# Kernel optimization log

Hardware: AMD Instinct MI355X
Metric: run time of the kernel (lower is better)

Reference implementation:

```python
import jax, jax.numpy as jnp
import numpy as np
from jax import lax

H = 512
W = 512
KS = 9  # dilation and Gaussian kernel size
# OpenCV: sigma=0 -> sigma = 0.3*((ksize-1)*0.5 - 1) + 0.8 = 1.7 for ksize=9
_SIGMA = 0.3 * ((KS - 1) * 0.5 - 1.0) + 0.8
_g = np.exp(-0.5 * ((np.arange(KS) - (KS - 1) / 2.0) / _SIGMA) ** 2)
_g = (_g / _g.sum()).astype(np.float32)
GAUSS = jnp.asarray(_g)


def setup_inputs() -> dict:
    key = jax.random.key(0)
    k1, k2, k3 = jax.random.split(key, 3)
    B, N = 64, 13860
    eye = jnp.eye(4, dtype=jnp.float32)
    # near-identity camera matrices so points project on-screen
    V = eye + 0.02 * jax.random.normal(k1, (B, 4, 4), jnp.float32)
    P = eye + 0.02 * jax.random.normal(k2, (B, 4, 4), jnp.float32)
    xyz = jax.random.uniform(k3, (N, 3), jnp.float32, -0.9, 0.9)
    pts = jnp.concatenate([xyz, jnp.ones((N, 1), jnp.float32)], axis=1)
    return {"V_matrix": V, "P_matrix": P, "raw_base_points": pts}


def reference(V_matrix, P_matrix, raw_base_points):
    B = V_matrix.shape[0]
    VP = jnp.einsum('bij,bjk->bik', P_matrix, V_matrix)          # [B,4,4]
    tp = jnp.einsum('ni,bji->bnj', raw_base_points, VP)          # points @ VP^T -> [B,N,4]
    w = tp[..., 3:4]
    xyz = jnp.where(w != 0, tp[..., :3] / w, tp[..., :3])       # perspective divide
    sx = jnp.round((xyz[..., 0] + 1.0) * 0.5 * W).astype(jnp.int32)
    sy = jnp.round((1.0 - (xyz[..., 1] + 1.0) * 0.5) * H).astype(jnp.int32)
    valid = (sx >= 0) & (sx < W) & (sy >= 0) & (sy < H)
    flat = jnp.where(valid, sy * W + sx, -1)                     # -1 -> dropped by scatter

    def splat(f):  # point splat: 255 at hit pixels (this is the inverted image)
        return jnp.zeros(H * W, jnp.float32).at[f].set(255.0, mode='drop').reshape(H, W)

    img = jax.vmap(splat)(flat)                                  # [B,H,W] in {0,255}
    dil = lax.reduce_window(img, -jnp.inf, lax.max, (1, KS, KS), (1, 1, 1), 'SAME')
    # 9x9 Gaussian blur, separable, BORDER_REFLECT_101 (OpenCV default)
    pad = jnp.pad(dil, ((0, 0), (KS // 2, KS // 2), (KS // 2, KS // 2)), mode='reflect')
    x = pad[:, None]                                             # [B,1,H+8,W+8]
    sm = lax.conv_general_dilated(x, GAUSS.reshape(1, 1, KS, 1), (1, 1), 'VALID')
    sm = lax.conv_general_dilated(sm, GAUSS.reshape(1, 1, 1, KS), (1, 1), 'VALID')[:, 0]
    # threshold(smoothed > 100) -> 255, then /255 -> {0,1}
    mask = (jnp.round(sm) > 100.0).astype(jnp.float32)           # [B,H,W]
    return jnp.broadcast_to(mask[:, None], (B, 3, H, W))
```

## Files before the change

kernel.cpp:

```cpp
#include <hip/hip_runtime.h>
#include <math.h>
#include <stdint.h>

#define HH 512
#define WW 512
#define BB 64
#define NP 13860
#define WPR 16
#define IMG_WORDS (BB * HH * WPR)

struct GaussW { float g[9]; };

__device__ __forceinline__ int reflect_idx(int i) {
    if (i < 0) i = -i;
    if (i > 511) i = 1022 - i;
    return i;
}

__global__ __launch_bounds__(256)
void zero_kernel(uint4* __restrict__ p) {
    p[blockIdx.x * 256 + threadIdx.x] = make_uint4(0u, 0u, 0u, 0u);
}

__global__ __launch_bounds__(256)
void splat_kernel(const float* __restrict__ V,
                  const float* __restrict__ P,
                  const float* __restrict__ pts,
                  unsigned int* __restrict__ gbm) {
    __shared__ float VP[4][4];
    const int b = blockIdx.y;
    const int t = threadIdx.x;
    if (t < 16) {
        const int i = t >> 2, k = t & 3;
        const float* Pb = P + b * 16;
        const float* Vb = V + b * 16;
        float a = __fmul_rn(Pb[i*4+0], Vb[0*4+k]);
        a = __fmaf_rn(Pb[i*4+1], Vb[1*4+k], a);
        a = __fmaf_rn(Pb[i*4+2], Vb[2*4+k], a);
        a = __fmaf_rn(Pb[i*4+3], Vb[3*4+k], a);
        VP[i][k] = a;
    }
    __syncthreads();
    const int n = blockIdx.x * 256 + t;
    if (n >= NP) return;
    const float4 p = ((const float4*)pts)[n];
    float tp0, tp1, tp3;
    {
        float a = __fmul_rn(p.x, VP[0][0]);
        a = __fmaf_rn(p.y, VP[0][1], a);
        a = __fmaf_rn(p.z, VP[0][2], a);
        a = __fmaf_rn(p.w, VP[0][3], a);
        tp0 = a;
    }
    {
        float a = __fmul_rn(p.x, VP[1][0]);
        a = __fmaf_rn(p.y, VP[1][1], a);
        a = __fmaf_rn(p.z, VP[1][2], a);
        a = __fmaf_rn(p.w, VP[1][3], a);
        tp1 = a;
    }
    {
        float a = __fmul_rn(p.x, VP[3][0]);
        a = __fmaf_rn(p.y, VP[3][1], a);
        a = __fmaf_rn(p.z, VP[3][2], a);
        a = __fmaf_rn(p.w, VP[3][3], a);
        tp3 = a;
    }
    const float w = tp3;
    const float x = (w != 0.f) ? (tp0 / w) : tp0;
    const float y = (w != 0.f) ? (tp1 / w) : tp1;
    const float sxf = rintf(__fmul_rn(__fmul_rn(__fadd_rn(x, 1.f), 0.5f), 512.f));
    const float tmp = __fmul_rn(__fadd_rn(y, 1.f), 0.5f);
    const float syf = rintf(__fmul_rn(__fsub_rn(1.f, tmp), 512.f));
    int sx, sy;
    if (sxf >= 0.f && sxf < 512.f && syf >= 0.f && syf < 512.f) {
        sx = (int)sxf; sy = (int)syf;
    } else {
        sx = 511; sy = 511;
    }
    atomicOr(&gbm[(b * HH + sy) * WPR + (sx >> 5)], 1u << (sx & 31));
}

__global__ __launch_bounds__(256)
void hdil_kernel(const unsigned int* __restrict__ in,
                 unsigned int* __restrict__ out) {
    const int idx = blockIdx.x * 256 + threadIdx.x;
    const int wx = idx & (WPR - 1);
    const unsigned int w  = in[idx];
    const unsigned int wl = (wx > 0)       ? in[idx - 1] : 0u;
    const unsigned int wr = (wx < WPR - 1) ? in[idx + 1] : 0u;
    unsigned int hd = w;
#pragma unroll
    for (int k = 1; k <= 4; ++k) {
        hd |= (w << k) | (wl >> (32 - k));
        hd |= (w >> k) | (wr << (32 - k));
    }
    out[idx] = hd;
}

__global__ __launch_bounds__(256)
void vdil_kernel(const unsigned int* __restrict__ in,
                 unsigned int* __restrict__ out) {
    const int idx = blockIdx.x * 256 + threadIdx.x;
    const int b   = idx / (HH * WPR);
    const int rem = idx - b * (HH * WPR);
    const int r   = rem >> 4;
    const int wx  = rem & (WPR - 1);
    const int lo = (r - 4 > 0) ? r - 4 : 0;
    const int hi = (r + 4 < HH - 1) ? r + 4 : HH - 1;
    const unsigned int* base = in + b * HH * WPR + wx;
    unsigned int acc = 0u;
    for (int rr = lo; rr <= hi; ++rr) acc |= base[rr * WPR];
    out[idx] = acc;
}

__global__ __launch_bounds__(256)
void tile_kernel(const unsigned int* __restrict__ gdil,
                 float* __restrict__ out, GaussW gw) {
    __shared__ float lut[512];

    const int b  = blockIdx.z;
    const int x0 = blockIdx.x * 64;
    const int y0 = blockIdx.y * 64;
    const int tx = threadIdx.x;
    const int ty = threadIdx.y;
    const int tid = ty * 16 + tx;

    for (int e = tid; e < 512; e += 256) {
        float acc = 0.f;
#pragma unroll
        for (int dy = 0; dy < 9; ++dy) {
            const float val = ((e >> dy) & 1) ? 255.f : 0.f;
            acc = __fmaf_rn(gw.g[dy], val, acc);
        }
        lut[e] = acc;
    }
    __syncthreads();

    const unsigned int* gb = gdil + b * HH * WPR;
    const int c0 = 4 * tx;

    int rk[12];
    const int rbase = y0 + 4 * ty - 4;
#pragma unroll
    for (int k = 0; k < 12; ++k)
        rk[k] = reflect_idx(rbase + k) * WPR;

    const bool colRef = (x0 == 0 && tx == 0) || (x0 == 448 && tx == 15);

    int mode = 2;
    unsigned int v12[12];

    if (!colRef) {
        const int colA = x0 + c0 - 4;
        const int wA = colA >> 5;
        const int w2 = (wA + 1 < WPR) ? wA + 1 : WPR - 1;
        const int sh = colA & 31;
        unsigned int e12[12], fOr = 0u, fAnd = 0xFFFu;
#pragma unroll
        for (int k = 0; k < 12; ++k) {
            const unsigned long long cat =
                (((unsigned long long)gb[rk[k] + w2]) << 32) |
                (unsigned long long)gb[rk[k] + wA];
            e12[k] = (unsigned int)(cat >> sh) & 0xFFFu;
            fOr |= e12[k]; fAnd &= e12[k];
        }
        if (fOr == 0u)           mode = 0;
        else if (fAnd == 0xFFFu) mode = 1;
        else {
#pragma unroll
            for (int j = 0; j < 12; ++j) {
                unsigned int v = 0u;
#pragma unroll
                for (int k = 0; k < 12; ++k)
                    v |= ((e12[k] >> j) & 1u) << k;
                v12[j] = v;
            }
        }
    } else {
        const int wsel = (x0 == 0) ? 0 : WPR - 1;
        unsigned int d[12];
#pragma unroll
        for (int k = 0; k < 12; ++k) d[k] = gb[rk[k] + wsel];
#pragma unroll
        for (int j = 0; j < 12; ++j) {
            const int col = reflect_idx(x0 + c0 - 4 + j);
            const int shc = col & 31;
            unsigned int v = 0u;
#pragma unroll
            for (int k = 0; k < 12; ++k)
                v |= ((d[k] >> shc) & 1u) << k;
            v12[j] = v;
        }
    }

#pragma unroll
    for (int r = 0; r < 4; ++r) {
        float4 mq;
        float* mp = (float*)&mq;
        if (mode == 0) {
            mq = make_float4(0.f, 0.f, 0.f, 0.f);
        } else if (mode == 1) {
            mq = make_float4(1.f, 1.f, 1.f, 1.f);
        } else {
            float f[12];
#pragma unroll
            for (int j = 0; j < 12; ++j)
                f[j] = lut[(v12[j] >> r) & 0x1FFu];
#pragma unroll
            for (int q = 0; q < 4; ++q) {
                float acc = 0.f;
#pragma unroll
                for (int dx = 0; dx < 9; ++dx)
                    acc = __fmaf_rn(gw.g[dx], f[q + dx], acc);
                mp[q] = (rintf(acc) > 100.f) ? 1.f : 0.f;
            }
        }
        const int yq = y0 + 4 * ty + r, xq = x0 + c0;
        float* o = out + ((size_t)(b * 3) * HH + yq) * WW + xq;
        *(float4*)(o)                       = mq;
        *(float4*)(o + (size_t)HH * WW)     = mq;
        *(float4*)(o + (size_t)2 * HH * WW) = mq;
    }
}

extern "C" void kernel_launch(void* const* d_in, const int* in_sizes, int n_in,
                              void* d_out, int out_size, void* d_ws, size_t ws_size,
                              hipStream_t stream) {
    const float* V   = (const float*)d_in[0];
    const float* P   = (const float*)d_in[1];
    const float* pts = (const float*)d_in[2];
    float* out = (float*)d_out;
    unsigned int* buf0 = (unsigned int*)d_ws;
    unsigned int* buf1 = buf0 + IMG_WORDS;

    const double sigma = 0.3 * ((9 - 1) * 0.5 - 1.0) + 0.8;
    double gd[9];
    for (int i = 0; i < 9; ++i) {
        const double t = ((double)i - 4.0) / sigma;
        gd[i] = exp(-0.5 * (t * t));
    }
    double s = ((gd[0] + gd[1]) + (gd[2] + gd[3])) + ((gd[4] + gd[5]) + (gd[6] + gd[7]));
    s += gd[8];
    GaussW gw;
    for (int i = 0; i < 9; ++i) gw.g[i] = (float)(gd[i] / s);

    zero_kernel<<<IMG_WORDS / 4 / 256, 256, 0, stream>>>((uint4*)buf0);
    splat_kernel<<<dim3((NP + 255) / 256, BB), 256, 0, stream>>>(V, P, pts, buf0);
    hdil_kernel<<<IMG_WORDS / 256, 256, 0, stream>>>(buf0, buf1);
    vdil_kernel<<<IMG_WORDS / 256, 256, 0, stream>>>(buf1, buf0);
    tile_kernel<<<dim3(8, 8, BB), dim3(16, 16), 0, stream>>>(buf0, out, gw);
}
```

Before: 91.41 us.

## Split mask computation into bitmask pass and nontemporal float expansion kernel

The tile kernel now writes the thresholded mask as a packed bitmask via atomicOr into a zeroed buffer instead of storing three float channels directly. A new expand kernel reads the bitmask and writes the 3-channel float output with nontemporal vector stores, 64 bytes per thread. The intent is to get streaming, well-coalesced output writes and to skip all-zero tiles early in the mask pass. The cost is two extra launches (a zero pass and the expand), atomics, and an extra round trip through the bitmask buffer.

Measured after the change: 362.8 us. +296.9%, slower.

```diff
diff --git a/kernel.cpp b/kernel.cpp
--- a/kernel.cpp
+++ b/kernel.cpp
@@ -8,6 +8,8 @@
 #define NP 13860
 #define WPR 16
 #define IMG_WORDS (BB * HH * WPR)
+
+typedef float vfloat4 __attribute__((ext_vector_type(4)));
 
 struct GaussW { float g[9]; };
 
@@ -115,8 +117,8 @@
 }
 
 __global__ __launch_bounds__(256)
-void tile_kernel(const unsigned int* __restrict__ gdil,
-                 float* __restrict__ out, GaussW gw) {
+void mask_kernel(const unsigned int* __restrict__ gdil,
+                 unsigned int* __restrict__ mb, GaussW gw) {
     __shared__ float lut[512];
 
     const int b  = blockIdx.z;
@@ -194,33 +196,57 @@
         }
     }
 
+    if (mode == 0) return;
+
+    const int xq0  = x0 + c0;
+    const int wdst = (b * HH) * WPR + (xq0 >> 5);
+    const int bsh  = xq0 & 31;
 #pragma unroll
     for (int r = 0; r < 4; ++r) {
-        float4 mq;
-        float* mp = (float*)&mq;
-        if (mode == 0) {
-            mq = make_float4(0.f, 0.f, 0.f, 0.f);
-        } else if (mode == 1) {
-            mq = make_float4(1.f, 1.f, 1.f, 1.f);
+        unsigned int nib;
+        if (mode == 1) {
+            nib = 0xFu;
         } else {
             float f[12];
 #pragma unroll
             for (int j = 0; j < 12; ++j)
                 f[j] = lut[(v12[j] >> r) & 0x1FFu];
+            nib = 0u;
 #pragma unroll
             for (int q = 0; q < 4; ++q) {
                 float acc = 0.f;
 #pragma unroll
                 for (int dx = 0; dx < 9; ++dx)
                     acc = __fmaf_rn(gw.g[dx], f[q + dx], acc);
-                mp[q] = (rintf(acc) > 100.f) ? 1.f : 0.f;
+                if (rintf(acc) > 100.f) nib |= (1u << q);
             }
-        }
-        const int yq = y0 + 4 * ty + r, xq = x0 + c0;
-        float* o = out + ((size_t)(b * 3) * HH + yq) * WW + xq;
-        *(float4*)(o)                       = mq;
-        *(float4*)(o + (size_t)HH * WW)     = mq;
-        *(float4*)(o + (size_t)2 * HH * WW) = mq;
+            if (nib == 0u) continue;
+        }
+        const int yq = y0 + 4 * ty + r;
+        atomicOr(&mb[wdst + yq * WPR], nib << bsh);
+    }
+}
+
+__global__ __launch_bounds__(256)
+void expand_kernel(const unsigned int* __restrict__ mb,
+                   float* __restrict__ out) {
+    const int c   = blockIdx.x * 256 + threadIdx.x;
+    const int y   = c >> 5;
+    const int x16 = c & 31;
+    const int b   = blockIdx.z;
+    const int ch  = blockIdx.y;
+
+    const unsigned int word = mb[(b * HH + y) * WPR + (x16 >> 1)];
+    const unsigned int bits = (word >> ((x16 & 1) * 16)) & 0xFFFFu;
+
+    float* o = out + (((size_t)(b * 3 + ch) * HH + y) * WW) + x16 * 16;
+#pragma unroll
+    for (int v = 0; v < 4; ++v) {
+        vfloat4 q;
+#pragma unroll
+        for (int i = 0; i < 4; ++i)
+            q[i] = ((bits >> (4 * v + i)) & 1u) ? 1.f : 0.f;
+        __builtin_nontemporal_store(q, (vfloat4*)(o + 4 * v));
     }
 }
 
@@ -249,5 +275,7 @@
     splat_kernel<<<dim3((NP + 255) / 256, BB), 256, 0, stream>>>(V, P, pts, buf0);
     hdil_kernel<<<IMG_WORDS / 256, 256, 0, stream>>>(buf0, buf1);
     vdil_kernel<<<IMG_WORDS / 256, 256, 0, stream>>>(buf1, buf0);
-    tile_kernel<<<dim3(8, 8, BB), dim3(16, 16), 0, stream>>>(buf0, out, gw);
-}
+    zero_kernel<<<IMG_WORDS / 4 / 256, 256, 0, stream>>>((uint4*)buf1);
+    mask_kernel<<<dim3(8, 8, BB), dim3(16, 16), 0, stream>>>(buf0, buf1, gw);
+    expand_kernel<<<dim3(64, 3, BB), 256, 0, stream>>>(buf1, out);
+}
```
